# Kernel tuning notes

Measured on AMD Instinct MI355X. Metric: run time of the kernel, lower is better.

Reference implementation:

```python
import jax, jax.numpy as jnp
import numpy as np

N_NODES = 256
COND = 64
ARCH = [256, 512, 1024]
E = N_NODES * (N_NODES - 1) // 2  # 32640 upper-triangular edges
OUT = 2 * E                        # 65280 final-layer width
B = 512
CUTOFF = 0.0
TAU = 1.0


def _make_params(key, dims):
    ws, bs = [], []
    for i, (din, dout) in enumerate(zip(dims[:-1], dims[1:])):
        k = jax.random.fold_in(key, i)
        kw, kb = jax.random.split(k)
        ws.append(jax.random.normal(kw, (din, dout), jnp.float32) * 0.02)
        bs.append(jax.random.normal(kb, (dout,), jnp.float32) * 0.02)
    return ws, bs


def setup_inputs() -> dict:
    key = jax.random.key(0)
    kx, kg, kbig, ksmall = jax.random.split(key, 4)
    x = jax.random.normal(kx, (B, COND), jnp.float32)
    gumbel = jax.random.gumbel(kg, (B, E, 2), jnp.float32)
    dims = [COND] + ARCH + [OUT]
    bw, bb = _make_params(kbig, dims)
    sw, sb = _make_params(ksmall, dims)
    inp = {"x": x, "gumbel": gumbel}
    for i in range(4):
        inp[f"bw{i}"] = bw[i]; inp[f"bb{i}"] = bb[i]
        inp[f"sw{i}"] = sw[i]; inp[f"sb{i}"] = sb[i]
    return inp


def _expert_adj(x, ws, bs, gumbel):
    # MLP: relu on all but last layer
    h = x
    for w, b in zip(ws[:-1], bs[:-1]):
        h = jax.nn.relu(h @ w + b)
    logits = (h @ ws[-1] + bs[-1]).reshape(x.shape[0], E, 2)
    # hard gumbel-softmax (straight-through), tau=1
    g = (logits + gumbel) / TAU
    y_soft = jax.nn.softmax(g, axis=-1)
    y_hard = jax.nn.one_hot(jnp.argmax(g, axis=-1), 2, dtype=y_soft.dtype)
    y = y_hard + y_soft - jax.lax.stop_gradient(y_soft)
    x0 = y[:, :, 0]  # [B, E]
    iu, ju = jnp.triu_indices(N_NODES, k=1)
    adj = jnp.zeros((x.shape[0], N_NODES, N_NODES), x0.dtype)
    adj = adj.at[:, iu, ju].set(x0)
    return adj + jnp.swapaxes(adj, 1, 2)


def reference(x, gumbel,
              bw0, bb0, bw1, bb1, bw2, bb2, bw3, bb3,
              sw0, sb0, sw1, sb1, sw2, sb2, sw3, sb3):
    big_ws, big_bs = [bw0, bw1, bw2, bw3], [bb0, bb1, bb2, bb3]
    small_ws, small_bs = [sw0, sw1, sw2, sw3], [sb0, sb1, sb2, sb3]
    adj_big = _expert_adj(x, big_ws, big_bs, gumbel)
    adj_small = _expert_adj(x, small_ws, small_bs, gumbel)
    mask_big = x[:, 0] > CUTOFF  # [B]
    out = jnp.where(mask_big[:, None, None], adj_big, adj_small)
    return out
```

## Files before the change

kernel.cpp:

```cpp
#include <hip/hip_runtime.h>

#define N_NODES 256
#define COND    64
#define E_PAIRS 32640
#define OUTCOLS 65280
#define BATCH   512
#define SLOTS   576
#define D1      256
#define D2      512
#define D3      1024

__global__ void k0_sort(const float* __restrict__ x, int* __restrict__ meta,
                        int* __restrict__ borig) {
    __shared__ int wc[9];
    int t = threadIdx.x;
    if (t < SLOTS) borig[t] = -1;
    int m = 0;
    if (t < BATCH) m = (x[t * COND] > 0.0f) ? 1 : 0;
    unsigned long long bm = __ballot(m);
    int wave = t >> 6;
    int lane = t & 63;
    int lanePre = __popcll(bm & ((1ull << lane) - 1ull));
    if (lane == 0) wc[wave] = __popcll(bm);
    __syncthreads();
    int nbig = 0, preBig = 0;
    #pragma unroll
    for (int w = 0; w < 8; ++w) {
        int c = wc[w];
        if (w < wave) preBig += c;
        nbig += c;
    }
    int S = (nbig + 63) & ~63;
    if (t < BATCH) {
        int onesBefore = preBig + lanePre;
        int slot = m ? onesBefore : (S + (t - onesBefore));
        borig[slot] = t;
    }
    if (t == 0) meta[0] = S;
}

template <bool GATHER, int K, int DOUT>
__global__ __launch_bounds__(256) void k1_gemm(
    const float* __restrict__ in,
    const float* __restrict__ wbig, const float* __restrict__ bbig,
    const float* __restrict__ wsml, const float* __restrict__ bsml,
    const int* __restrict__ meta, const int* __restrict__ borig,
    float* __restrict__ out) {
    __shared__ float hs[16][64 + 4];
    __shared__ float wt[16][64 + 4];
    int tid = threadIdx.x;
    int by = blockIdx.x;
    int bx = blockIdx.y;
    int r0 = by * 64;
    int cb = bx * 64;
    int S = meta[0];
    bool big = (r0 < S);
    const float* w = big ? wbig : wsml;
    const float* bias = big ? bbig : bsml;

    int lm = tid >> 2;
    int lq = tid & 3;
    int wk = tid >> 4;
    int wc = (tid & 15) * 4;

    int tm = tid >> 4;
    int tn = tid & 15;

    const float* hrow;
    if (GATHER) {
        int b = borig[r0 + lm];
        hrow = (b >= 0) ? &in[(size_t)b * K] : (const float*)0;
    } else {
        hrow = &in[(size_t)(r0 + lm) * K];
    }

    float acc[4][4];
    #pragma unroll
    for (int i = 0; i < 4; ++i)
        #pragma unroll
        for (int j = 0; j < 4; ++j) acc[i][j] = 0.f;

    for (int k0 = 0; k0 < K; k0 += 16) {
        float4 hv = make_float4(0.f, 0.f, 0.f, 0.f);
        if (!GATHER || hrow) hv = *(const float4*)&hrow[k0 + lq * 4];
        float4 wv = *(const float4*)&w[(size_t)(k0 + wk) * DOUT + cb + wc];
        __syncthreads();
        hs[lq * 4 + 0][lm] = hv.x;
        hs[lq * 4 + 1][lm] = hv.y;
        hs[lq * 4 + 2][lm] = hv.z;
        hs[lq * 4 + 3][lm] = hv.w;
        *(float4*)&wt[wk][wc] = wv;
        __syncthreads();
        #pragma unroll
        for (int kk = 0; kk < 16; ++kk) {
            float4 a  = *(const float4*)&hs[kk][tm * 4];
            float4 bf = *(const float4*)&wt[kk][tn * 4];
            acc[0][0] = fmaf(a.x, bf.x, acc[0][0]);
            acc[0][1] = fmaf(a.x, bf.y, acc[0][1]);
            acc[0][2] = fmaf(a.x, bf.z, acc[0][2]);
            acc[0][3] = fmaf(a.x, bf.w, acc[0][3]);
            acc[1][0] = fmaf(a.y, bf.x, acc[1][0]);
            acc[1][1] = fmaf(a.y, bf.y, acc[1][1]);
            acc[1][2] = fmaf(a.y, bf.z, acc[1][2]);
            acc[1][3] = fmaf(a.y, bf.w, acc[1][3]);
            acc[2][0] = fmaf(a.z, bf.x, acc[2][0]);
            acc[2][1] = fmaf(a.z, bf.y, acc[2][1]);
            acc[2][2] = fmaf(a.z, bf.z, acc[2][2]);
            acc[2][3] = fmaf(a.z, bf.w, acc[2][3]);
            acc[3][0] = fmaf(a.w, bf.x, acc[3][0]);
            acc[3][1] = fmaf(a.w, bf.y, acc[3][1]);
            acc[3][2] = fmaf(a.w, bf.z, acc[3][2]);
            acc[3][3] = fmaf(a.w, bf.w, acc[3][3]);
        }
    }

    float4 bv = *(const float4*)&bias[cb + tn * 4];
    #pragma unroll
    for (int i = 0; i < 4; ++i) {
        float4 o;
        o.x = fmaxf(acc[i][0] + bv.x, 0.f);
        o.y = fmaxf(acc[i][1] + bv.y, 0.f);
        o.z = fmaxf(acc[i][2] + bv.z, 0.f);
        o.w = fmaxf(acc[i][3] + bv.w, 0.f);
        *(float4*)&out[(size_t)(r0 + tm * 4 + i) * DOUT + cb + tn * 4] = o;
    }
}

#define BM   64
#define BNW  256
#define BND  128
#define BK   16
__global__ __launch_bounds__(256) void k2_logits(
    const float* __restrict__ hbuf,
    const float* __restrict__ bw3, const float* __restrict__ bb3,
    const float* __restrict__ sw3, const float* __restrict__ sb3,
    const float* __restrict__ gum,
    const int* __restrict__ meta, const int* __restrict__ borig,
    unsigned char* __restrict__ bits) {
    __shared__ float hs[BK][BM + 4];
    __shared__ float wt[BK][BND + 4];
    int tid = threadIdx.x;
    int by = blockIdx.x;
    int bx = blockIdx.y;
    int r0 = by * BM;
    int cb = bx * BNW;
    int S = meta[0];
    bool big = (r0 < S);
    const float* w3 = big ? bw3 : sw3;
    const float* b3 = big ? bb3 : sb3;

    int lm  = tid >> 2;
    int lq  = tid & 3;
    int wk  = tid >> 4;
    int wc  = (tid & 15) * 16;
    int wd  = (tid & 15) * 8;

    int tm = tid >> 5;
    int tn = tid & 31;

    float acc[8][4];
    #pragma unroll
    for (int i = 0; i < 8; ++i)
        #pragma unroll
        for (int j = 0; j < 4; ++j) acc[i][j] = 0.f;

    for (int k0 = 0; k0 < D3; k0 += BK) {
        float4 hv = *(const float4*)&hbuf[(size_t)(r0 + lm) * D3 + k0 + lq * 4];
        const float* wrow = &w3[(size_t)(k0 + wk) * OUTCOLS + cb + wc];
        float4 wv0 = *(const float4*)&wrow[0];
        float4 wv1 = *(const float4*)&wrow[4];
        float4 wv2 = *(const float4*)&wrow[8];
        float4 wv3 = *(const float4*)&wrow[12];
        __syncthreads();
        hs[lq * 4 + 0][lm] = hv.x;
        hs[lq * 4 + 1][lm] = hv.y;
        hs[lq * 4 + 2][lm] = hv.z;
        hs[lq * 4 + 3][lm] = hv.w;
        float4 d0, d1;
        d0.x = wv0.x - wv0.y;  d0.y = wv0.z - wv0.w;
        d0.z = wv1.x - wv1.y;  d0.w = wv1.z - wv1.w;
        d1.x = wv2.x - wv2.y;  d1.y = wv2.z - wv2.w;
        d1.z = wv3.x - wv3.y;  d1.w = wv3.z - wv3.w;
        *(float4*)&wt[wk][wd]     = d0;
        *(float4*)&wt[wk][wd + 4] = d1;
        __syncthreads();
        #pragma unroll
        for (int kk = 0; kk < BK; ++kk) {
            float4 a0 = *(const float4*)&hs[kk][tm * 8];
            float4 a1 = *(const float4*)&hs[kk][tm * 8 + 4];
            float4 bf = *(const float4*)&wt[kk][tn * 4];
            float am[8] = {a0.x, a0.y, a0.z, a0.w, a1.x, a1.y, a1.z, a1.w};
            float bn[4] = {bf.x, bf.y, bf.z, bf.w};
            #pragma unroll
            for (int i = 0; i < 8; ++i)
                #pragma unroll
                for (int j = 0; j < 4; ++j)
                    acc[i][j] = fmaf(am[i], bn[j], acc[i][j]);
        }
    }

    float4 bv0 = *(const float4*)&b3[cb + tn * 8];
    float4 bv1 = *(const float4*)&b3[cb + tn * 8 + 4];
    float bd0 = bv0.x - bv0.y;
    float bd1 = bv0.z - bv0.w;
    float bd2 = bv1.x - bv1.y;
    float bd3 = bv1.z - bv1.w;
    int ebase = bx * BND + tn * 4;
    #pragma unroll
    for (int i = 0; i < 8; ++i) {
        int slot = r0 + tm * 8 + i;
        int b = borig[slot];
        if (b < 0) continue;
        const float* gp = &gum[(size_t)b * OUTCOLS + (size_t)ebase * 2];
        float4 gv0 = *(const float4*)&gp[0];
        float4 gv1 = *(const float4*)&gp[4];
        uchar4 v;
        v.x = ((acc[i][0] + bd0) + (gv0.x - gv0.y) >= 0.f) ? 1 : 0;
        v.y = ((acc[i][1] + bd1) + (gv0.z - gv0.w) >= 0.f) ? 1 : 0;
        v.z = ((acc[i][2] + bd2) + (gv1.x - gv1.y) >= 0.f) ? 1 : 0;
        v.w = ((acc[i][3] + bd3) + (gv1.z - gv1.w) >= 0.f) ? 1 : 0;
        *(uchar4*)&bits[(size_t)b * E_PAIRS + ebase] = v;
    }
}

__global__ __launch_bounds__(256) void k3_expand(
    const unsigned char* __restrict__ bits, float* __restrict__ out) {
    __shared__ unsigned char L[64][68];
    const int ti_tab[10] = {0,0,0,0,1,1,1,2,2,3};
    const int tj_tab[10] = {0,1,2,3,1,2,3,2,3,3};
    int p = blockIdx.x;
    int b = blockIdx.y;
    int ti = ti_tab[p], tj = tj_tab[p];
    int t = threadIdx.x;

    {
        int r = t >> 2;
        int q = t & 3;
        int i = ti * 64 + r;
        long base = (long)b * E_PAIRS + (long)i * (511 - i) / 2 - i - 1;
        int j0 = tj * 64 + q * 16;
        #pragma unroll
        for (int k = 0; k < 16; ++k) {
            int j = j0 + k;
            unsigned char v = (j > i) ? bits[base + j] : (unsigned char)0;
            L[r][q * 16 + k] = v;
        }
    }
    __syncthreads();

    int h  = t >> 4;
    int w4 = (t & 15) * 4;

    {
        #pragma unroll
        for (int rr = 0; rr < 4; ++rr) {
            int ii = rr * 16 + h;
            int i_ = ti * 64 + ii;
            float4 v;
            if (ti == tj) {
                int jj;
                jj = w4 + 0; v.x = (jj > ii) ? (float)L[ii][jj] : (jj < ii ? (float)L[jj][ii] : 0.f);
                jj = w4 + 1; v.y = (jj > ii) ? (float)L[ii][jj] : (jj < ii ? (float)L[jj][ii] : 0.f);
                jj = w4 + 2; v.z = (jj > ii) ? (float)L[ii][jj] : (jj < ii ? (float)L[jj][ii] : 0.f);
                jj = w4 + 3; v.w = (jj > ii) ? (float)L[ii][jj] : (jj < ii ? (float)L[jj][ii] : 0.f);
            } else {
                v.x = (float)L[ii][w4 + 0];
                v.y = (float)L[ii][w4 + 1];
                v.z = (float)L[ii][w4 + 2];
                v.w = (float)L[ii][w4 + 3];
            }
            size_t o = (((size_t)b * 256 + i_) * 256) + tj * 64 + w4;
            *(float4*)&out[o] = v;
        }
    }

    if (ti != tj) {
        #pragma unroll
        for (int rr = 0; rr < 4; ++rr) {
            int jj = rr * 16 + h;
            int j_ = tj * 64 + jj;
            float4 v;
            v.x = (float)L[w4 + 0][jj];
            v.y = (float)L[w4 + 1][jj];
            v.z = (float)L[w4 + 2][jj];
            v.w = (float)L[w4 + 3][jj];
            size_t o = (((size_t)b * 256 + j_) * 256) + ti * 64 + w4;
            *(float4*)&out[o] = v;
        }
    }
}

extern "C" void kernel_launch(void* const* d_in, const int* in_sizes, int n_in,
                              void* d_out, int out_size, void* d_ws, size_t ws_size,
                              hipStream_t stream) {
    const float* x   = (const float*)d_in[0];
    const float* gum = (const float*)d_in[1];
    const float* bw0 = (const float*)d_in[2];  const float* bb0 = (const float*)d_in[3];
    const float* sw0 = (const float*)d_in[4];  const float* sb0 = (const float*)d_in[5];
    const float* bw1 = (const float*)d_in[6];  const float* bb1 = (const float*)d_in[7];
    const float* sw1 = (const float*)d_in[8];  const float* sb1 = (const float*)d_in[9];
    const float* bw2 = (const float*)d_in[10]; const float* bb2 = (const float*)d_in[11];
    const float* sw2 = (const float*)d_in[12]; const float* sb2 = (const float*)d_in[13];
    const float* bw3 = (const float*)d_in[14]; const float* bb3 = (const float*)d_in[15];
    const float* sw3 = (const float*)d_in[16]; const float* sb3 = (const float*)d_in[17];

    char* ws = (char*)d_ws;
    int*   meta  = (int*)ws;
    int*   borig = (int*)(ws + 64);
    float* act1  = (float*)(ws + 4096);
    float* act2  = (float*)(ws + 4096 + 589824);
    float* hbuf  = (float*)(ws + 4096 + 589824 + 1179648);
    unsigned char* bits = (unsigned char*)(ws + 4194304);
    float* out = (float*)d_out;

    k0_sort<<<1, SLOTS, 0, stream>>>(x, meta, borig);
    k1_gemm<true,  COND, D1><<<dim3(9, D1 / 64), 256, 0, stream>>>(
        x,    bw0, bb0, sw0, sb0, meta, borig, act1);
    k1_gemm<false, D1,   D2><<<dim3(9, D2 / 64), 256, 0, stream>>>(
        act1, bw1, bb1, sw1, sb1, meta, borig, act2);
    k1_gemm<false, D2,   D3><<<dim3(9, D3 / 64), 256, 0, stream>>>(
        act2, bw2, bb2, sw2, sb2, meta, borig, hbuf);
    k2_logits<<<dim3(9, 255), 256, 0, stream>>>(hbuf, bw3, bb3, sw3, sb3, gum,
                                                meta, borig, bits);
    k3_expand<<<dim3(10, BATCH), 256, 0, stream>>>(bits, out);
}
```

Baseline: 1.078 ms.

## Use bf16x3 split MFMA for final logits GEMM with swizzled LDS and grid remap

```diff
diff --git a/kernel.cpp b/kernel.cpp
--- a/kernel.cpp
+++ b/kernel.cpp
@@ -9,6 +9,18 @@
 #define D1      256
 #define D2      512
 #define D3      1024
+
+typedef __attribute__((ext_vector_type(8))) short bf16x8;
+typedef __attribute__((ext_vector_type(4))) float f32x4;
+
+static __device__ __forceinline__ unsigned short f2bf(float f) {
+    unsigned int u = __float_as_uint(f);
+    u += 0x7FFF + ((u >> 16) & 1);
+    return (unsigned short)(u >> 16);
+}
+static __device__ __forceinline__ float bf2f(unsigned short h) {
+    return __uint_as_float(((unsigned int)h) << 16);
+}
 
 __global__ void k0_sort(const float* __restrict__ x, int* __restrict__ meta,
                         int* __restrict__ borig) {
@@ -39,13 +51,15 @@
     if (t == 0) meta[0] = S;
 }
 
-template <bool GATHER, int K, int DOUT>
+template <bool GATHER, int K, int DOUT, bool SPLIT>
 __global__ __launch_bounds__(256) void k1_gemm(
     const float* __restrict__ in,
     const float* __restrict__ wbig, const float* __restrict__ bbig,
     const float* __restrict__ wsml, const float* __restrict__ bsml,
     const int* __restrict__ meta, const int* __restrict__ borig,
-    float* __restrict__ out) {
+    float* __restrict__ out,
+    unsigned short* __restrict__ hb0, unsigned short* __restrict__ hb1,
+    unsigned short* __restrict__ hb2) {
     __shared__ float hs[16][64 + 4];
     __shared__ float wt[16][64 + 4];
     int tid = threadIdx.x;
@@ -117,109 +131,173 @@
     float4 bv = *(const float4*)&bias[cb + tn * 4];
     #pragma unroll
     for (int i = 0; i < 4; ++i) {
-        float4 o;
-        o.x = fmaxf(acc[i][0] + bv.x, 0.f);
-        o.y = fmaxf(acc[i][1] + bv.y, 0.f);
-        o.z = fmaxf(acc[i][2] + bv.z, 0.f);
-        o.w = fmaxf(acc[i][3] + bv.w, 0.f);
-        *(float4*)&out[(size_t)(r0 + tm * 4 + i) * DOUT + cb + tn * 4] = o;
-    }
-}
-
-#define BM   64
-#define BNW  256
-#define BND  128
-#define BK   16
-__global__ __launch_bounds__(256) void k2_logits(
-    const float* __restrict__ hbuf,
+        float o[4];
+        o[0] = fmaxf(acc[i][0] + bv.x, 0.f);
+        o[1] = fmaxf(acc[i][1] + bv.y, 0.f);
+        o[2] = fmaxf(acc[i][2] + bv.z, 0.f);
+        o[3] = fmaxf(acc[i][3] + bv.w, 0.f);
+        size_t off = (size_t)(r0 + tm * 4 + i) * DOUT + cb + tn * 4;
+        if (SPLIT) {
+            ushort4 s0, s1, s2;
+            unsigned short* p0[4] = {&s0.x, &s0.y, &s0.z, &s0.w};
+            unsigned short* p1[4] = {&s1.x, &s1.y, &s1.z, &s1.w};
+            unsigned short* p2[4] = {&s2.x, &s2.y, &s2.z, &s2.w};
+            #pragma unroll
+            for (int j = 0; j < 4; ++j) {
+                unsigned short a0 = f2bf(o[j]);
+                float r1v = o[j] - bf2f(a0);
+                unsigned short a1 = f2bf(r1v);
+                float r2v = r1v - bf2f(a1);
+                unsigned short a2 = f2bf(r2v);
+                *p0[j] = a0; *p1[j] = a1; *p2[j] = a2;
+            }
+            *(ushort4*)&hb0[off] = s0;
+            *(ushort4*)&hb1[off] = s1;
+            *(ushort4*)&hb2[off] = s2;
+        } else {
+            float4 ov;
+            ov.x = o[0]; ov.y = o[1]; ov.z = o[2]; ov.w = o[3];
+            *(float4*)&out[off] = ov;
+        }
+    }
+}
+
+__global__ __launch_bounds__(256) void k2_mfma(
+    const unsigned short* __restrict__ hb0, const unsigned short* __restrict__ hb1,
+    const unsigned short* __restrict__ hb2,
     const float* __restrict__ bw3, const float* __restrict__ bb3,
     const float* __restrict__ sw3, const float* __restrict__ sb3,
     const float* __restrict__ gum,
     const int* __restrict__ meta, const int* __restrict__ borig,
     unsigned char* __restrict__ bits) {
-    __shared__ float hs[BK][BM + 4];
-    __shared__ float wt[BK][BND + 4];
+    __shared__ unsigned short As[3][64][32];
+    __shared__ unsigned short Bs[3][128][32];
+
     int tid = threadIdx.x;
-    int by = blockIdx.x;
-    int bx = blockIdx.y;
-    int r0 = by * BM;
-    int cb = bx * BNW;
+    int wgid = blockIdx.x;
+    int xr  = wgid & 7;
+    int s_  = wgid >> 3;
+    int by  = s_ % 9;
+    int q   = s_ / 9;
+    int bx  = q * 8 + xr;
+    if (bx >= 255) return;
+
+    int r0 = by * 64;
+    int cb = bx * 256;
+    int db = bx * 128;
     int S = meta[0];
     bool big = (r0 < S);
     const float* w3 = big ? bw3 : sw3;
     const float* b3 = big ? bb3 : sb3;
 
-    int lm  = tid >> 2;
-    int lq  = tid & 3;
-    int wk  = tid >> 4;
-    int wc  = (tid & 15) * 16;
-    int wd  = (tid & 15) * 8;
-
-    int tm = tid >> 5;
-    int tn = tid & 31;
-
-    float acc[8][4];
+    int lane = tid & 63;
+    int wid  = tid >> 6;
+    int l15  = lane & 15;
+    int lg   = lane >> 4;
+
+    int arow = tid >> 2;
+    int aq   = (tid & 3) * 8;
+    int bkk  = tid >> 3;
+    int bc8  = tid & 7;
+    int c3w  = bc8 & 3;
+    int kidx = (bkk & 7) | (((bkk >> 3) ^ c3w) << 3);
+
+    f32x4 acc[4][2];
     #pragma unroll
-    for (int i = 0; i < 8; ++i)
-        #pragma unroll
-        for (int j = 0; j < 4; ++j) acc[i][j] = 0.f;
-
-    for (int k0 = 0; k0 < D3; k0 += BK) {
-        float4 hv = *(const float4*)&hbuf[(size_t)(r0 + lm) * D3 + k0 + lq * 4];
-        const float* wrow = &w3[(size_t)(k0 + wk) * OUTCOLS + cb + wc];
-        float4 wv0 = *(const float4*)&wrow[0];
-        float4 wv1 = *(const float4*)&wrow[4];
-        float4 wv2 = *(const float4*)&wrow[8];
-        float4 wv3 = *(const float4*)&wrow[12];
+    for (int m = 0; m < 4; ++m)
+        #pragma unroll
+        for (int n = 0; n < 2; ++n) acc[m][n] = (f32x4)0.f;
+
+    const unsigned short* ha0 = &hb0[(size_t)(r0 + arow) * D3 + aq];
+    const unsigned short* ha1 = &hb1[(size_t)(r0 + arow) * D3 + aq];
+    const unsigned short* ha2 = &hb2[(size_t)(r0 + arow) * D3 + aq];
+
+    for (int k0 = 0; k0 < D3; k0 += 32) {
+        uint4 av0 = *(const uint4*)&ha0[k0];
+        uint4 av1 = *(const uint4*)&ha1[k0];
+        uint4 av2 = *(const uint4*)&ha2[k0];
+        const float* wr = &w3[(size_t)(k0 + bkk) * OUTCOLS + cb + bc8 * 32];
+        float4 wv0 = *(const float4*)&wr[0];
+        float4 wv1 = *(const float4*)&wr[4];
+        float4 wv2 = *(const float4*)&wr[8];
+        float4 wv3 = *(const float4*)&wr[12];
+        float4 wv4 = *(const float4*)&wr[16];
+        float4 wv5 = *(const float4*)&wr[20];
+        float4 wv6 = *(const float4*)&wr[24];
+        float4 wv7 = *(const float4*)&wr[28];
         __syncthreads();
-        hs[lq * 4 + 0][lm] = hv.x;
-        hs[lq * 4 + 1][lm] = hv.y;
-        hs[lq * 4 + 2][lm] = hv.z;
-        hs[lq * 4 + 3][lm] = hv.w;
-        float4 d0, d1;
-        d0.x = wv0.x - wv0.y;  d0.y = wv0.z - wv0.w;
-        d0.z = wv1.x - wv1.y;  d0.w = wv1.z - wv1.w;
-        d1.x = wv2.x - wv2.y;  d1.y = wv2.z - wv2.w;
-        d1.z = wv3.x - wv3.y;  d1.w = wv3.z - wv3.w;
-        *(float4*)&wt[wk][wd]     = d0;
-        *(float4*)&wt[wk][wd + 4] = d1;
+        *(uint4*)&As[0][arow][aq] = av0;
+        *(uint4*)&As[1][arow][aq] = av1;
+        *(uint4*)&As[2][arow][aq] = av2;
+        {
+            float d[16] = {
+                wv0.x - wv0.y, wv0.z - wv0.w, wv1.x - wv1.y, wv1.z - wv1.w,
+                wv2.x - wv2.y, wv2.z - wv2.w, wv3.x - wv3.y, wv3.z - wv3.w,
+                wv4.x - wv4.y, wv4.z - wv4.w, wv5.x - wv5.y, wv5.z - wv5.w,
+                wv6.x - wv6.y, wv6.z - wv6.w, wv7.x - wv7.y, wv7.z - wv7.w };
+            #pragma unroll
+            for (int i = 0; i < 16; ++i) {
+                int colv = bc8 * 16 + i;
+                float dv = d[i];
+                unsigned short d0 = f2bf(dv);
+                float r1v = dv - bf2f(d0);
+                unsigned short d1 = f2bf(r1v);
+                float r2v = r1v - bf2f(d1);
+                unsigned short d2 = f2bf(r2v);
+                Bs[0][colv][kidx] = d0;
+                Bs[1][colv][kidx] = d1;
+                Bs[2][colv][kidx] = d2;
+            }
+        }
         __syncthreads();
-        #pragma unroll
-        for (int kk = 0; kk < BK; ++kk) {
-            float4 a0 = *(const float4*)&hs[kk][tm * 8];
-            float4 a1 = *(const float4*)&hs[kk][tm * 8 + 4];
-            float4 bf = *(const float4*)&wt[kk][tn * 4];
-            float am[8] = {a0.x, a0.y, a0.z, a0.w, a1.x, a1.y, a1.z, a1.w};
-            float bn[4] = {bf.x, bf.y, bf.z, bf.w};
+        bf16x8 af0[4], af1[4], af2[4];
+        #pragma unroll
+        for (int m = 0; m < 4; ++m) {
+            af0[m] = *(const bf16x8*)&As[0][m * 16 + l15][lg * 8];
+            af1[m] = *(const bf16x8*)&As[1][m * 16 + l15][lg * 8];
+            af2[m] = *(const bf16x8*)&As[2][m * 16 + l15][lg * 8];
+        }
+        bf16x8 bf0[2], bf1[2], bf2v[2];
+        #pragma unroll
+        for (int n = 0; n < 2; ++n) {
+            int col = wid * 32 + n * 16 + l15;
+            int kb  = (lg ^ ((col >> 4) & 3)) * 8;
+            bf0[n]  = *(const bf16x8*)&Bs[0][col][kb];
+            bf1[n]  = *(const bf16x8*)&Bs[1][col][kb];
+            bf2v[n] = *(const bf16x8*)&Bs[2][col][kb];
+        }
+        #pragma unroll
+        for (int m = 0; m < 4; ++m)
             #pragma unroll
-            for (int i = 0; i < 8; ++i)
-                #pragma unroll
-                for (int j = 0; j < 4; ++j)
-                    acc[i][j] = fmaf(am[i], bn[j], acc[i][j]);
-        }
-    }
-
-    float4 bv0 = *(const float4*)&b3[cb + tn * 8];
-    float4 bv1 = *(const float4*)&b3[cb + tn * 8 + 4];
-    float bd0 = bv0.x - bv0.y;
-    float bd1 = bv0.z - bv0.w;
-    float bd2 = bv1.x - bv1.y;
-    float bd3 = bv1.z - bv1.w;
-    int ebase = bx * BND + tn * 4;
+            for (int n = 0; n < 2; ++n) {
+                f32x4 c = acc[m][n];
+                c = __builtin_amdgcn_mfma_f32_16x16x32_bf16(af0[m], bf0[n],  c, 0, 0, 0);
+                c = __builtin_amdgcn_mfma_f32_16x16x32_bf16(af0[m], bf1[n],  c, 0, 0, 0);
+                c = __builtin_amdgcn_mfma_f32_16x16x32_bf16(af1[m], bf0[n],  c, 0, 0, 0);
+                c = __builtin_amdgcn_mfma_f32_16x16x32_bf16(af1[m], bf1[n],  c, 0, 0, 0);
+                c = __builtin_amdgcn_mfma_f32_16x16x32_bf16(af0[m], bf2v[n], c, 0, 0, 0);
+                c = __builtin_amdgcn_mfma_f32_16x16x32_bf16(af2[m], bf0[n],  c, 0, 0, 0);
+                acc[m][n] = c;
+            }
+    }
+
     #pragma unroll
-    for (int i = 0; i < 8; ++i) {
-        int slot = r0 + tm * 8 + i;
-        int b = borig[slot];
-        if (b < 0) continue;
-        const float* gp = &gum[(size_t)b * OUTCOLS + (size_t)ebase * 2];
-        float4 gv0 = *(const float4*)&gp[0];
-        float4 gv1 = *(const float4*)&gp[4];
-        uchar4 v;
-        v.x = ((acc[i][0] + bd0) + (gv0.x - gv0.y) >= 0.f) ? 1 : 0;
-        v.y = ((acc[i][1] + bd1) + (gv0.z - gv0.w) >= 0.f) ? 1 : 0;
-        v.z = ((acc[i][2] + bd2) + (gv1.x - gv1.y) >= 0.f) ? 1 : 0;
-        v.w = ((acc[i][3] + bd3) + (gv1.z - gv1.w) >= 0.f) ? 1 : 0;
-        *(uchar4*)&bits[(size_t)b * E_PAIRS + ebase] = v;
+    for (int n = 0; n < 2; ++n) {
+        int colg = db + wid * 32 + n * 16 + l15;
+        float2 bv = *(const float2*)&b3[2 * colg];
+        float bd = bv.x - bv.y;
+        #pragma unroll
+        for (int m = 0; m < 4; ++m) {
+            #pragma unroll
+            for (int r = 0; r < 4; ++r) {
+                int slot = r0 + m * 16 + lg * 4 + r;
+                int b = borig[slot];
+                if (b < 0) continue;
+                float2 gv = *(const float2*)&gum[(size_t)b * OUTCOLS + 2 * colg];
+                float g = acc[m][n][r] + bd + (gv.x - gv.y);
+                bits[(size_t)b * E_PAIRS + colg] = (g >= 0.f) ? 1 : 0;
+            }
+        }
     }
 }
 
@@ -308,19 +386,21 @@
     int*   meta  = (int*)ws;
     int*   borig = (int*)(ws + 64);
     float* act1  = (float*)(ws + 4096);
-    float* act2  = (float*)(ws + 4096 + 589824);
-    float* hbuf  = (float*)(ws + 4096 + 589824 + 1179648);
-    unsigned char* bits = (unsigned char*)(ws + 4194304);
+    float* act2  = (float*)(ws + 593920);
+    unsigned short* hb0 = (unsigned short*)(ws + 1773568);
+    unsigned short* hb1 = (unsigned short*)(ws + 2953216);
+    unsigned short* hb2 = (unsigned short*)(ws + 4132864);
+    unsigned char* bits = (unsigned char*)(ws + 5312512);
     float* out = (float*)d_out;
 
     k0_sort<<<1, SLOTS, 0, stream>>>(x, meta, borig);
-    k1_gemm<true,  COND, D1><<<dim3(9, D1 / 64), 256, 0, stream>>>(
-        x,    bw0, bb0, sw0, sb0, meta, borig, act1);
-    k1_gemm<false, D1,   D2><<<dim3(9, D2 / 64), 256, 0, stream>>>(
-        act1, bw1, bb1, sw1, sb1, meta, borig, act2);
-    k1_gemm<false, D2,   D3><<<dim3(9, D3 / 64), 256, 0, stream>>>(
-        act2, bw2, bb2, sw2, sb2, meta, borig, hbuf);
-    k2_logits<<<dim3(9, 255), 256, 0, stream>>>(hbuf, bw3, bb3, sw3, sb3, gum,
-                                                meta, borig, bits);
+    k1_gemm<true,  COND, D1, false><<<dim3(9, D1 / 64), 256, 0, stream>>>(
+        x,    bw0, bb0, sw0, sb0, meta, borig, act1, 0, 0, 0);
+    k1_gemm<false, D1,   D2, false><<<dim3(9, D2 / 64), 256, 0, stream>>>(
+        act1, bw1, bb1, sw1, sb1, meta, borig, act2, 0, 0, 0);
+    k1_gemm<false, D2,   D3, true><<<dim3(9, D3 / 64), 256, 0, stream>>>(
+        act2, bw2, bb2, sw2, sb2, meta, borig, (float*)0, hb0, hb1, hb2);
+    k2_mfma<<<2304, 256, 0, stream>>>(hb0, hb1, hb2, bw3, bb3, sw3, sb3, gum,
+                                      meta, borig, bits);
     k3_expand<<<dim3(10, BATCH), 256, 0, stream>>>(bits, out);
 }
```

After: 1.050 ms. -2.6%, faster.
